# Kernel tuning notes

Measured on AMD Instinct MI355X. Metric: run time of the kernel, lower is better.

The kernel has to match this reference:

```python
import jax, jax.numpy as jnp
import numpy as np

B, C, W, H, D = 2, 256, 32, 32, 32
CH = C // 2  # 128
LN_EPS = 1e-5


def _spatial_pool(x, wm, bm):
    # x: [B,C,W,H,D]; wm: [C]; bm: scalar. 1x1x1 conv C->1 == channel dot.
    b, c = x.shape[0], x.shape[1]
    xf = x.reshape(b, c, -1)                       # [B,C,N]
    mask = jnp.einsum('bcn,c->bn', xf, wm) + bm    # [B,N]
    attn = jax.nn.softmax(mask, axis=1)            # softmax over spatial N
    return jnp.einsum('bcn,bn->bc', xf, attn)      # [B,C] weighted-sum pool


def _channel_add(ctx, w1, b1, g, be, w2, b2):
    # 1x1 conv C->C/2, LayerNorm over C/2, ReLU, 1x1 conv C/2->C
    h = ctx @ w1.T + b1                            # [B,CH]
    mu = jnp.mean(h, axis=-1, keepdims=True)
    var = jnp.mean((h - mu) ** 2, axis=-1, keepdims=True)
    h = (h - mu) * jax.lax.rsqrt(var + LN_EPS) * g + be
    h = jax.nn.relu(h)
    return h @ w2.T + b2                           # [B,C]


def setup_inputs() -> dict:
    key = jax.random.key(0)
    ks = jax.random.split(key, 20)
    s = 0.02
    d = {
        'preds_S': jax.random.normal(ks[0], (B, C, W, H, D), jnp.float32),
        'preds_T': jax.random.normal(ks[1], (B, C, W, H, D), jnp.float32),
        'wm_s': jax.random.normal(ks[2], (C,), jnp.float32) * s,
        'bm_s': jnp.zeros((), jnp.float32),
        'wm_t': jax.random.normal(ks[3], (C,), jnp.float32) * s,
        'bm_t': jnp.zeros((), jnp.float32),
        'w1_s': jax.random.normal(ks[4], (CH, C), jnp.float32) * s,
        'b1_s': jnp.zeros((CH,), jnp.float32),
        'g_s': jnp.ones((CH,), jnp.float32),
        'be_s': jnp.zeros((CH,), jnp.float32),
        'w2_s': jax.random.normal(ks[5], (C, CH), jnp.float32) * s,
        'b2_s': jnp.zeros((C,), jnp.float32),
        'w1_t': jax.random.normal(ks[6], (CH, C), jnp.float32) * s,
        'b1_t': jnp.zeros((CH,), jnp.float32),
        'g_t': jnp.ones((CH,), jnp.float32),
        'be_t': jnp.zeros((CH,), jnp.float32),
        'w2_t': jax.random.normal(ks[7], (C, CH), jnp.float32) * s,
        'b2_t': jnp.zeros((C,), jnp.float32),
    }
    return d


def reference(preds_S, preds_T, wm_s, bm_s, wm_t, bm_t,
              w1_s, b1_s, g_s, be_s, w2_s, b2_s,
              w1_t, b1_t, g_t, be_t, w2_t, b2_t):
    ctx_s = _spatial_pool(preds_S, wm_s, bm_s)     # [B,C]
    ctx_t = _spatial_pool(preds_T, wm_t, bm_t)
    add_s = _channel_add(ctx_s, w1_s, b1_s, g_s, be_s, w2_s, b2_s)  # [B,C]
    add_t = _channel_add(ctx_t, w1_t, b1_t, g_t, be_t, w2_t, b2_t)
    out_s = preds_S + add_s[:, :, None, None, None]
    out_t = preds_T + add_t[:, :, None, None, None]
    diff = out_s - out_t
    return jnp.sum(diff * diff) / preds_S.shape[0]
```

## Files before the change

kernel.cpp:

```cpp
#include <hip/hip_runtime.h>
#include <math.h>

#define Bc   2
#define Cc   256
#define Nn   32768
#define CHc  128
#define LN_EPS 1e-5f

#define TN    64
#define TPB   512
#define NQ    16
#define CG    32
#define CPG   8
#define GRIDX (Nn / TN)

__global__ __launch_bounds__(TPB, 2) void gc_fused(
    const float* __restrict__ S, const float* __restrict__ T,
    const float* __restrict__ wms, const float* __restrict__ bms,
    const float* __restrict__ wmt, const float* __restrict__ bmt,
    float* __restrict__ ctxnum,
    float* __restrict__ rowsum,
    float* __restrict__ den,
    float* __restrict__ sumsq) {
  const int b    = blockIdx.y;
  const int tid  = threadIdx.x;
  const int nq   = tid & (NQ - 1);
  const int cg   = tid >> 4;
  const int wv   = tid >> 6;
  const int lane = tid & 63;
  const int c0   = cg * CPG;
  const int n0   = blockIdx.x * TN + nq * 4;

  __shared__ float4 mredw[2][8][NQ];
  __shared__ float  cred[Cc * 17];
  __shared__ float  sqred[8];
  __shared__ float  denred[2][NQ];

  const float bS = bms[0];
  const float bT = bmt[0];

  const float* Sp = S + ((size_t)b * Cc + c0) * Nn + n0;
  const float* Tp = T + ((size_t)b * Cc + c0) * Nn + n0;

  float4 s4[CPG], t4[CPG];
#pragma unroll
  for (int i = 0; i < CPG; ++i) s4[i] = *(const float4*)(Sp + (size_t)i * Nn);
#pragma unroll
  for (int i = 0; i < CPG; ++i) t4[i] = *(const float4*)(Tp + (size_t)i * Nn);

  float wS[CPG], wT[CPG];
#pragma unroll
  for (int i = 0; i < CPG; ++i) { wS[i] = wms[c0 + i]; wT[i] = wmt[c0 + i]; }

  float4 ms = make_float4(0.f, 0.f, 0.f, 0.f);
  float4 mt = make_float4(0.f, 0.f, 0.f, 0.f);
#pragma unroll
  for (int i = 0; i < CPG; ++i) {
    ms.x += wS[i] * s4[i].x; ms.y += wS[i] * s4[i].y;
    ms.z += wS[i] * s4[i].z; ms.w += wS[i] * s4[i].w;
    mt.x += wT[i] * t4[i].x; mt.y += wT[i] * t4[i].y;
    mt.z += wT[i] * t4[i].z; mt.w += wT[i] * t4[i].w;
  }

#pragma unroll
  for (int m = 16; m <= 32; m <<= 1) {
    ms.x += __shfl_xor(ms.x, m); ms.y += __shfl_xor(ms.y, m);
    ms.z += __shfl_xor(ms.z, m); ms.w += __shfl_xor(ms.w, m);
    mt.x += __shfl_xor(mt.x, m); mt.y += __shfl_xor(mt.y, m);
    mt.z += __shfl_xor(mt.z, m); mt.w += __shfl_xor(mt.w, m);
  }
  if (lane < NQ) { mredw[0][wv][nq] = ms; mredw[1][wv][nq] = mt; }

  __syncthreads();

  float4 Ms = make_float4(0.f, 0.f, 0.f, 0.f);
  float4 Mt = make_float4(0.f, 0.f, 0.f, 0.f);
#pragma unroll
  for (int w = 0; w < 8; ++w) {
    const float4 a = mredw[0][w][nq];
    Ms.x += a.x; Ms.y += a.y; Ms.z += a.z; Ms.w += a.w;
    const float4 c = mredw[1][w][nq];
    Mt.x += c.x; Mt.y += c.y; Mt.z += c.z; Mt.w += c.w;
  }
  float4 es, et;
  es.x = __expf(Ms.x + bS); es.y = __expf(Ms.y + bS);
  es.z = __expf(Ms.z + bS); es.w = __expf(Ms.w + bS);
  et.x = __expf(Mt.x + bT); et.y = __expf(Mt.y + bT);
  et.z = __expf(Mt.z + bT); et.w = __expf(Mt.w + bT);

  if (tid < NQ) {
    denred[0][tid] = es.x + es.y + es.z + es.w;
    denred[1][tid] = et.x + et.y + et.z + et.w;
  }

#pragma unroll
  for (int i = 0; i < CPG; ++i)
    cred[(c0 + i) * 17 + nq] =
        s4[i].x * es.x + s4[i].y * es.y + s4[i].z * es.z + s4[i].w * es.w;
  __syncthreads();
  if (tid < Cc) {
    float a = 0.f;
#pragma unroll
    for (int k = 0; k < NQ; ++k) a += cred[tid * 17 + k];
    atomicAdd(&ctxnum[((size_t)0 * Bc + b) * Cc + tid], a);
  } else if (tid == Cc + 1) {
    float a = 0.f, c = 0.f;
#pragma unroll
    for (int k = 0; k < NQ; ++k) { a += denred[0][k]; c += denred[1][k]; }
    atomicAdd(&den[0 * Bc + b], a);
    atomicAdd(&den[1 * Bc + b], c);
  }
  __syncthreads();

#pragma unroll
  for (int i = 0; i < CPG; ++i)
    cred[(c0 + i) * 17 + nq] =
        t4[i].x * et.x + t4[i].y * et.y + t4[i].z * et.z + t4[i].w * et.w;
  __syncthreads();
  if (tid < Cc) {
    float c = 0.f;
#pragma unroll
    for (int k = 0; k < NQ; ++k) c += cred[tid * 17 + k];
    atomicAdd(&ctxnum[((size_t)1 * Bc + b) * Cc + tid], c);
  }
  __syncthreads();

  float sq = 0.f;
#pragma unroll
  for (int i = 0; i < CPG; ++i) {
    const float dx = s4[i].x - t4[i].x, dy = s4[i].y - t4[i].y;
    const float dz = s4[i].z - t4[i].z, dw = s4[i].w - t4[i].w;
    cred[(c0 + i) * 17 + nq] = dx + dy + dz + dw;
    sq += dx * dx + dy * dy + dz * dz + dw * dw;
  }
#pragma unroll
  for (int m = 1; m < 64; m <<= 1) sq += __shfl_xor(sq, m);
  if (lane == 0) sqred[wv] = sq;
  __syncthreads();
  if (tid < Cc) {
    float r = 0.f;
#pragma unroll
    for (int k = 0; k < NQ; ++k) r += cred[tid * 17 + k];
    atomicAdd(&rowsum[(size_t)b * Cc + tid], r);
  } else if (tid == Cc) {
    float v = 0.f;
#pragma unroll
    for (int w = 0; w < 8; ++w) v += sqred[w];
    atomicAdd(sumsq, v);
  }
}

__global__ __launch_bounds__(1024) void gc_k4a_mlp(
    const float* __restrict__ ctxr, const float* __restrict__ den,
    const float* __restrict__ w1s, const float* __restrict__ b1s,
    const float* __restrict__ gs,  const float* __restrict__ bes,
    const float* __restrict__ w2s, const float* __restrict__ b2s,
    const float* __restrict__ w1t, const float* __restrict__ b1t,
    const float* __restrict__ gt,  const float* __restrict__ bet,
    const float* __restrict__ w2t, const float* __restrict__ b2t,
    float* __restrict__ addv) {
  const int tt  = blockIdx.x >> 1;
  const int b   = blockIdx.x & 1;
  const int tid = threadIdx.x;

  const float* w1 = tt ? w1t : w1s;
  const float* b1 = tt ? b1t : b1s;
  const float* g  = tt ? gt  : gs;
  const float* be = tt ? bet : bes;
  const float* w2 = tt ? w2t : w2s;
  const float* b2 = tt ? b2t : b2s;

  __shared__ float cxs[Cc];
  __shared__ float part[1024];
  __shared__ float hbuf[CHc];
  __shared__ float hr[CHc];
  __shared__ float2 red2[128];
  __shared__ float mu_s, rstd_s;

  if (tid < Cc)
    cxs[tid] = ctxr[((size_t)tt * Bc + b) * Cc + tid] / den[tt * Bc + b];
  __syncthreads();

  {
    const int j = tid >> 3, s = tid & 7;
    const float* wr = w1 + j * Cc + s * 32;
    const float4* cx4 = (const float4*)(cxs + s * 32);
    float acc = 0.f;
#pragma unroll
    for (int k = 0; k < 8; ++k) {
      const float4 w = *(const float4*)(wr + k * 4);
      const float4 x = cx4[k];
      acc += w.x * x.x + w.y * x.y + w.z * x.z + w.w * x.w;
    }
    part[tid] = acc;
  }
  __syncthreads();
  if (tid < CHc) {
    float h = b1[tid];
#pragma unroll
    for (int q = 0; q < 8; ++q) h += part[tid * 8 + q];
    hbuf[tid] = h;
  }
  __syncthreads();

  if (tid < CHc) {
    const float v = hbuf[tid];
    red2[tid] = make_float2(v, v * v);
  }
  __syncthreads();
  for (int s = 64; s > 0; s >>= 1) {
    if (tid < s) {
      red2[tid].x += red2[tid + s].x;
      red2[tid].y += red2[tid + s].y;
    }
    __syncthreads();
  }
  if (tid == 0) {
    const float mu = red2[0].x / (float)CHc;
    const float var = red2[0].y / (float)CHc - mu * mu;
    mu_s = mu;
    rstd_s = rsqrtf(var + LN_EPS);
  }
  __syncthreads();
  if (tid < CHc) {
    const float v = (hbuf[tid] - mu_s) * rstd_s * g[tid] + be[tid];
    hr[tid] = v > 0.f ? v : 0.f;
  }
  __syncthreads();

  {
    const int c = tid >> 2, q = tid & 3;
    const float* wr = w2 + c * CHc + q * 32;
    const float4* h4 = (const float4*)(hr + q * 32);
    float acc = 0.f;
#pragma unroll
    for (int k = 0; k < 8; ++k) {
      const float4 w = *(const float4*)(wr + k * 4);
      const float4 x = h4[k];
      acc += w.x * x.x + w.y * x.y + w.z * x.z + w.w * x.w;
    }
    part[tid] = acc;
  }
  __syncthreads();
  if (tid < Cc) {
    float acc = b2[tid];
#pragma unroll
    for (int q = 0; q < 4; ++q) acc += part[tid * 4 + q];
    addv[((size_t)tt * Bc + b) * Cc + tid] = acc;
  }
}

__global__ __launch_bounds__(256) void gc_k4b_final(
    const float* __restrict__ addv, const float* __restrict__ rowsum,
    const float* __restrict__ sumsq, float* __restrict__ out) {
  const int tid = threadIdx.x;
  __shared__ float red[256];
  float part = 0.f;
  for (int job = tid; job < Bc * Cc; job += 256) {
    const int c = job & (Cc - 1);
    const int b = job >> 8;
    const float delta = addv[((size_t)0 * Bc + b) * Cc + c] -
                        addv[((size_t)1 * Bc + b) * Cc + c];
    part += 2.f * delta * rowsum[(size_t)b * Cc + c] +
            (float)Nn * delta * delta;
  }
  red[tid] = part;
  __syncthreads();
  for (int s = 128; s > 0; s >>= 1) {
    if (tid < s) red[tid] += red[tid + s];
    __syncthreads();
  }
  if (tid == 0) out[0] = (red[0] + sumsq[0]) / (float)Bc;
}

extern "C" void kernel_launch(void* const* d_in, const int* in_sizes, int n_in,
                              void* d_out, int out_size, void* d_ws,
                              size_t ws_size, hipStream_t stream) {
  const float* S   = (const float*)d_in[0];
  const float* T   = (const float*)d_in[1];
  const float* wms = (const float*)d_in[2];
  const float* bms = (const float*)d_in[3];
  const float* wmt = (const float*)d_in[4];
  const float* bmt = (const float*)d_in[5];
  const float* w1s = (const float*)d_in[6];
  const float* b1s = (const float*)d_in[7];
  const float* gs  = (const float*)d_in[8];
  const float* bes = (const float*)d_in[9];
  const float* w2s = (const float*)d_in[10];
  const float* b2s = (const float*)d_in[11];
  const float* w1t = (const float*)d_in[12];
  const float* b1t = (const float*)d_in[13];
  const float* gt  = (const float*)d_in[14];
  const float* bet = (const float*)d_in[15];
  const float* w2t = (const float*)d_in[16];
  const float* b2t = (const float*)d_in[17];
  float* out = (float*)d_out;

  float* ws     = (float*)d_ws;
  float* ctxnum = ws;
  float* rowsum = ctxnum + 2 * Bc * Cc;
  float* den    = rowsum + Bc * Cc;
  float* sumsq  = den + 4;
  float* addv   = sumsq + 1;

  hipMemsetAsync(d_ws, 0, (2 * Bc * Cc + Bc * Cc + 4 + 1) * sizeof(float),
                 stream);

  gc_fused<<<dim3(GRIDX, Bc), TPB, 0, stream>>>(S, T, wms, bms, wmt, bmt,
                                                ctxnum, rowsum, den, sumsq);
  gc_k4a_mlp<<<4, 1024, 0, stream>>>(ctxnum, den, w1s, b1s, gs, bes, w2s, b2s,
                                     w1t, b1t, gt, bet, w2t, b2t, addv);
  gc_k4b_final<<<1, 256, 0, stream>>>(addv, rowsum, sumsq, out);
}
```

Before: 207.9 us.

## Stage tiles via global_load_lds, loop per block, replace atomics with partial buffers

The main kernel now copies S and T tiles straight into LDS with global_load_lds. Each block loops over four spatial tiles and keeps its per-channel partial sums in registers. Each block then writes one row of partials to a workspace buffer, and the MLP and final kernels reduce those rows. This removes the global atomics and the workspace memset, cutting contention and a launch. The cost is synchronous LDS staging with no double buffering, a few more shuffles per channel, and serial reductions over 256 rows in small single-block kernels.

```diff
diff --git a/kernel.cpp b/kernel.cpp
--- a/kernel.cpp
+++ b/kernel.cpp
@@ -7,151 +7,153 @@
 #define CHc  128
 #define LN_EPS 1e-5f
 
-#define TN    64
-#define TPB   512
-#define NQ    16
-#define CG    32
-#define CPG   8
-#define GRIDX (Nn / TN)
-
-__global__ __launch_bounds__(TPB, 2) void gc_fused(
+#define TN    32
+#define TPT   4
+#define TPB   256
+#define NQ    8
+#define NB    (Nn / (TN * TPT))
+#define PR    772
+
+__device__ __forceinline__ void load_lds16(const float* g, float* l) {
+  __builtin_amdgcn_global_load_lds(
+      (const __attribute__((address_space(1))) void*)g,
+      (__attribute__((address_space(3))) void*)l, 16, 0, 0);
+}
+
+__global__ __launch_bounds__(TPB, 2) void gc_main(
     const float* __restrict__ S, const float* __restrict__ T,
     const float* __restrict__ wms, const float* __restrict__ bms,
     const float* __restrict__ wmt, const float* __restrict__ bmt,
-    float* __restrict__ ctxnum,
-    float* __restrict__ rowsum,
-    float* __restrict__ den,
-    float* __restrict__ sumsq) {
+    float* __restrict__ P) {
   const int b    = blockIdx.y;
+  const int blk  = blockIdx.x;
   const int tid  = threadIdx.x;
   const int nq   = tid & (NQ - 1);
-  const int cg   = tid >> 4;
+  const int cgrp = tid >> 3;
   const int wv   = tid >> 6;
   const int lane = tid & 63;
-  const int c0   = cg * CPG;
-  const int n0   = blockIdx.x * TN + nq * 4;
-
-  __shared__ float4 mredw[2][8][NQ];
-  __shared__ float  cred[Cc * 17];
-  __shared__ float  sqred[8];
-  __shared__ float  denred[2][NQ];
+  const int c0   = cgrp * 8;
+
+  __shared__ float  tileS[Cc * TN];
+  __shared__ float  tileT[Cc * TN];
+  __shared__ float4 mredw[2][4][NQ];
+  __shared__ float  sqred[4];
 
   const float bS = bms[0];
   const float bT = bmt[0];
 
-  const float* Sp = S + ((size_t)b * Cc + c0) * Nn + n0;
-  const float* Tp = T + ((size_t)b * Cc + c0) * Nn + n0;
-
-  float4 s4[CPG], t4[CPG];
-#pragma unroll
-  for (int i = 0; i < CPG; ++i) s4[i] = *(const float4*)(Sp + (size_t)i * Nn);
-#pragma unroll
-  for (int i = 0; i < CPG; ++i) t4[i] = *(const float4*)(Tp + (size_t)i * Nn);
-
-  float wS[CPG], wT[CPG];
-#pragma unroll
-  for (int i = 0; i < CPG; ++i) { wS[i] = wms[c0 + i]; wT[i] = wmt[c0 + i]; }
-
-  float4 ms = make_float4(0.f, 0.f, 0.f, 0.f);
-  float4 mt = make_float4(0.f, 0.f, 0.f, 0.f);
-#pragma unroll
-  for (int i = 0; i < CPG; ++i) {
-    ms.x += wS[i] * s4[i].x; ms.y += wS[i] * s4[i].y;
-    ms.z += wS[i] * s4[i].z; ms.w += wS[i] * s4[i].w;
-    mt.x += wT[i] * t4[i].x; mt.y += wT[i] * t4[i].y;
-    mt.z += wT[i] * t4[i].z; mt.w += wT[i] * t4[i].w;
-  }
-
-#pragma unroll
-  for (int m = 16; m <= 32; m <<= 1) {
-    ms.x += __shfl_xor(ms.x, m); ms.y += __shfl_xor(ms.y, m);
-    ms.z += __shfl_xor(ms.z, m); ms.w += __shfl_xor(ms.w, m);
-    mt.x += __shfl_xor(mt.x, m); mt.y += __shfl_xor(mt.y, m);
-    mt.z += __shfl_xor(mt.z, m); mt.w += __shfl_xor(mt.w, m);
-  }
-  if (lane < NQ) { mredw[0][wv][nq] = ms; mredw[1][wv][nq] = mt; }
-
-  __syncthreads();
-
-  float4 Ms = make_float4(0.f, 0.f, 0.f, 0.f);
-  float4 Mt = make_float4(0.f, 0.f, 0.f, 0.f);
-#pragma unroll
-  for (int w = 0; w < 8; ++w) {
-    const float4 a = mredw[0][w][nq];
-    Ms.x += a.x; Ms.y += a.y; Ms.z += a.z; Ms.w += a.w;
-    const float4 c = mredw[1][w][nq];
-    Mt.x += c.x; Mt.y += c.y; Mt.z += c.z; Mt.w += c.w;
-  }
-  float4 es, et;
-  es.x = __expf(Ms.x + bS); es.y = __expf(Ms.y + bS);
-  es.z = __expf(Ms.z + bS); es.w = __expf(Ms.w + bS);
-  et.x = __expf(Mt.x + bT); et.y = __expf(Mt.y + bT);
-  et.z = __expf(Mt.z + bT); et.w = __expf(Mt.w + bT);
-
-  if (tid < NQ) {
-    denred[0][tid] = es.x + es.y + es.z + es.w;
-    denred[1][tid] = et.x + et.y + et.z + et.w;
-  }
-
-#pragma unroll
-  for (int i = 0; i < CPG; ++i)
-    cred[(c0 + i) * 17 + nq] =
-        s4[i].x * es.x + s4[i].y * es.y + s4[i].z * es.z + s4[i].w * es.w;
-  __syncthreads();
-  if (tid < Cc) {
-    float a = 0.f;
-#pragma unroll
-    for (int k = 0; k < NQ; ++k) a += cred[tid * 17 + k];
-    atomicAdd(&ctxnum[((size_t)0 * Bc + b) * Cc + tid], a);
-  } else if (tid == Cc + 1) {
-    float a = 0.f, c = 0.f;
-#pragma unroll
-    for (int k = 0; k < NQ; ++k) { a += denred[0][k]; c += denred[1][k]; }
-    atomicAdd(&den[0 * Bc + b], a);
-    atomicAdd(&den[1 * Bc + b], c);
-  }
-  __syncthreads();
-
-#pragma unroll
-  for (int i = 0; i < CPG; ++i)
-    cred[(c0 + i) * 17 + nq] =
-        t4[i].x * et.x + t4[i].y * et.y + t4[i].z * et.z + t4[i].w * et.w;
-  __syncthreads();
-  if (tid < Cc) {
-    float c = 0.f;
-#pragma unroll
-    for (int k = 0; k < NQ; ++k) c += cred[tid * 17 + k];
-    atomicAdd(&ctxnum[((size_t)1 * Bc + b) * Cc + tid], c);
-  }
-  __syncthreads();
-
-  float sq = 0.f;
-#pragma unroll
-  for (int i = 0; i < CPG; ++i) {
-    const float dx = s4[i].x - t4[i].x, dy = s4[i].y - t4[i].y;
-    const float dz = s4[i].z - t4[i].z, dw = s4[i].w - t4[i].w;
-    cred[(c0 + i) * 17 + nq] = dx + dy + dz + dw;
-    sq += dx * dx + dy * dy + dz * dz + dw * dw;
-  }
-#pragma unroll
-  for (int m = 1; m < 64; m <<= 1) sq += __shfl_xor(sq, m);
-  if (lane == 0) sqred[wv] = sq;
-  __syncthreads();
-  if (tid < Cc) {
-    float r = 0.f;
-#pragma unroll
-    for (int k = 0; k < NQ; ++k) r += cred[tid * 17 + k];
-    atomicAdd(&rowsum[(size_t)b * Cc + tid], r);
-  } else if (tid == Cc) {
-    float v = 0.f;
-#pragma unroll
-    for (int w = 0; w < 8; ++w) v += sqred[w];
-    atomicAdd(sumsq, v);
-  }
-}
-
-__global__ __launch_bounds__(1024) void gc_k4a_mlp(
-    const float* __restrict__ ctxr, const float* __restrict__ den,
+  float wSv[8], wTv[8];
+#pragma unroll
+  for (int i = 0; i < 8; ++i) { wSv[i] = wms[c0 + i]; wTv[i] = wmt[c0 + i]; }
+
+  float acc_cs = 0.f, acc_ct = 0.f, acc_rs = 0.f, acc_sq = 0.f;
+  float acc_dens = 0.f, acc_dent = 0.f;
+
+  const int r = lane >> 3, o = lane & 7;
+
+  for (int it = 0; it < TPT; ++it) {
+    const int n0 = (blk * TPT + it) * TN;
+
+#pragma unroll
+    for (int j = 0; j < 16; ++j) {
+      const int ttn = j >> 3;
+      const int cb  = (wv * 8 + (j & 7)) * 8;
+      const float* gp = (ttn ? T : S) +
+          ((size_t)(b * Cc + cb + r)) * Nn + n0 + o * 4;
+      float* lp = (ttn ? tileT : tileS) + cb * TN;
+      load_lds16(gp, lp);
+    }
+    __syncthreads();
+
+    const float4* tS4 = (const float4*)tileS;
+    const float4* tT4 = (const float4*)tileT;
+
+    float4 ms = make_float4(0.f, 0.f, 0.f, 0.f);
+    float4 mt = make_float4(0.f, 0.f, 0.f, 0.f);
+#pragma unroll
+    for (int i = 0; i < 8; ++i) {
+      const float4 s = tS4[(c0 + i) * NQ + nq];
+      const float4 t = tT4[(c0 + i) * NQ + nq];
+      ms.x += wSv[i] * s.x; ms.y += wSv[i] * s.y;
+      ms.z += wSv[i] * s.z; ms.w += wSv[i] * s.w;
+      mt.x += wTv[i] * t.x; mt.y += wTv[i] * t.y;
+      mt.z += wTv[i] * t.z; mt.w += wTv[i] * t.w;
+    }
+#pragma unroll
+    for (int m = 8; m <= 32; m <<= 1) {
+      ms.x += __shfl_xor(ms.x, m); ms.y += __shfl_xor(ms.y, m);
+      ms.z += __shfl_xor(ms.z, m); ms.w += __shfl_xor(ms.w, m);
+      mt.x += __shfl_xor(mt.x, m); mt.y += __shfl_xor(mt.y, m);
+      mt.z += __shfl_xor(mt.z, m); mt.w += __shfl_xor(mt.w, m);
+    }
+    if (lane < NQ) { mredw[0][wv][nq] = ms; mredw[1][wv][nq] = mt; }
+    __syncthreads();
+
+    float4 Ms = make_float4(0.f, 0.f, 0.f, 0.f);
+    float4 Mt = make_float4(0.f, 0.f, 0.f, 0.f);
+#pragma unroll
+    for (int w = 0; w < 4; ++w) {
+      const float4 a = mredw[0][w][nq];
+      Ms.x += a.x; Ms.y += a.y; Ms.z += a.z; Ms.w += a.w;
+      const float4 c = mredw[1][w][nq];
+      Mt.x += c.x; Mt.y += c.y; Mt.z += c.z; Mt.w += c.w;
+    }
+    float4 es, et;
+    es.x = __expf(Ms.x + bS); es.y = __expf(Ms.y + bS);
+    es.z = __expf(Ms.z + bS); es.w = __expf(Ms.w + bS);
+    et.x = __expf(Mt.x + bT); et.y = __expf(Mt.y + bT);
+    et.z = __expf(Mt.z + bT); et.w = __expf(Mt.w + bT);
+    if (cgrp == 0) {
+      acc_dens += es.x + es.y + es.z + es.w;
+      acc_dent += et.x + et.y + et.z + et.w;
+    }
+
+#pragma unroll
+    for (int i = 0; i < 8; ++i) {
+      const float4 s = tS4[(c0 + i) * NQ + nq];
+      const float4 t = tT4[(c0 + i) * NQ + nq];
+      float cs = s.x * es.x + s.y * es.y + s.z * es.z + s.w * es.w;
+      float ct = t.x * et.x + t.y * et.y + t.z * et.z + t.w * et.w;
+      const float dx = s.x - t.x, dy = s.y - t.y;
+      const float dz = s.z - t.z, dw = s.w - t.w;
+      float rs = dx + dy + dz + dw;
+      acc_sq += dx * dx + dy * dy + dz * dz + dw * dw;
+#pragma unroll
+      for (int m = 1; m <= 4; m <<= 1) {
+        cs += __shfl_xor(cs, m);
+        ct += __shfl_xor(ct, m);
+        rs += __shfl_xor(rs, m);
+      }
+      if (nq == i) { acc_cs += cs; acc_ct += ct; acc_rs += rs; }
+    }
+    __syncthreads();
+  }
+
+#pragma unroll
+  for (int m = 1; m < 64; m <<= 1) acc_sq += __shfl_xor(acc_sq, m);
+  if (lane == 0) sqred[wv] = acc_sq;
+  if (wv == 0) {
+#pragma unroll
+    for (int m = 1; m <= 4; m <<= 1) {
+      acc_dens += __shfl_xor(acc_dens, m);
+      acc_dent += __shfl_xor(acc_dent, m);
+    }
+  }
+  __syncthreads();
+
+  float* Prow = P + ((size_t)b * NB + blk) * PR;
+  Prow[tid]       = acc_cs;
+  Prow[Cc + tid]  = acc_ct;
+  Prow[2 * Cc + tid] = acc_rs;
+  if (tid == 0) {
+    Prow[768] = acc_dens;
+    Prow[769] = acc_dent;
+    Prow[770] = sqred[0] + sqred[1] + sqred[2] + sqred[3];
+  }
+}
+
+__global__ __launch_bounds__(1024) void gc_mlp(
+    const float* __restrict__ P,
     const float* __restrict__ w1s, const float* __restrict__ b1s,
     const float* __restrict__ gs,  const float* __restrict__ bes,
     const float* __restrict__ w2s, const float* __restrict__ b2s,
@@ -170,6 +172,8 @@
   const float* w2 = tt ? w2t : w2s;
   const float* b2 = tt ? b2t : b2s;
 
+  __shared__ float red4[4][Cc];
+  __shared__ float den4[4];
   __shared__ float cxs[Cc];
   __shared__ float part[1024];
   __shared__ float hbuf[CHc];
@@ -177,8 +181,23 @@
   __shared__ float2 red2[128];
   __shared__ float mu_s, rstd_s;
 
+  {
+    const int c = tid & (Cc - 1), gq = tid >> 8;
+    float v = 0.f;
+    for (int t = gq * 64; t < gq * 64 + 64; ++t)
+      v += P[((size_t)b * NB + t) * PR + tt * Cc + c];
+    red4[gq][c] = v;
+    if (tid < 4) {
+      float dv = 0.f;
+      for (int t = tid * 64; t < tid * 64 + 64; ++t)
+        dv += P[((size_t)b * NB + t) * PR + 768 + tt];
+      den4[tid] = dv;
+    }
+  }
+  __syncthreads();
   if (tid < Cc)
-    cxs[tid] = ctxr[((size_t)tt * Bc + b) * Cc + tid] / den[tt * Bc + b];
+    cxs[tid] = (red4[0][tid] + red4[1][tid] + red4[2][tid] + red4[3][tid]) /
+               (den4[0] + den4[1] + den4[2] + den4[3]);
   __syncthreads();
 
   {
@@ -250,27 +269,53 @@
   }
 }
 
-__global__ __launch_bounds__(256) void gc_k4b_final(
-    const float* __restrict__ addv, const float* __restrict__ rowsum,
-    const float* __restrict__ sumsq, float* __restrict__ out) {
+__global__ __launch_bounds__(1024) void gc_fin(
+    const float* __restrict__ P, const float* __restrict__ addv,
+    float* __restrict__ out) {
   const int tid = threadIdx.x;
-  __shared__ float red[256];
+  __shared__ float rs2[2][2][Cc];
+  __shared__ float red[1024];
+  __shared__ float sq_tot;
+
+  {
+    const int c = tid & (Cc - 1), b = (tid >> 8) & 1, h = tid >> 9;
+    float v = 0.f;
+    for (int t = h * 128; t < h * 128 + 128; ++t)
+      v += P[((size_t)b * NB + t) * PR + 2 * Cc + c];
+    rs2[h][b][c] = v;
+  }
+  {
+    float sqv = 0.f;
+    if (tid < 512) {
+      const int b = tid >> 8, t = tid & (NB - 1);
+      sqv = P[((size_t)b * NB + t) * PR + 770];
+    }
+    red[tid] = sqv;
+  }
+  __syncthreads();
+  for (int s = 512; s > 0; s >>= 1) {
+    if (tid < s) red[tid] += red[tid + s];
+    __syncthreads();
+  }
+  if (tid == 0) sq_tot = red[0];
+  __syncthreads();
+
   float part = 0.f;
-  for (int job = tid; job < Bc * Cc; job += 256) {
-    const int c = job & (Cc - 1);
-    const int b = job >> 8;
+  if (tid < Bc * Cc) {
+    const int c = tid & (Cc - 1);
+    const int b = tid >> 8;
     const float delta = addv[((size_t)0 * Bc + b) * Cc + c] -
                         addv[((size_t)1 * Bc + b) * Cc + c];
-    part += 2.f * delta * rowsum[(size_t)b * Cc + c] +
-            (float)Nn * delta * delta;
+    const float rsum = rs2[0][b][c] + rs2[1][b][c];
+    part = 2.f * delta * rsum + (float)Nn * delta * delta;
   }
   red[tid] = part;
   __syncthreads();
-  for (int s = 128; s > 0; s >>= 1) {
+  for (int s = 512; s > 0; s >>= 1) {
     if (tid < s) red[tid] += red[tid + s];
     __syncthreads();
   }
-  if (tid == 0) out[0] = (red[0] + sumsq[0]) / (float)Bc;
+  if (tid == 0) out[0] = (red[0] + sq_tot) / (float)Bc;
 }
 
 extern "C" void kernel_launch(void* const* d_in, const int* in_sizes, int n_in,
@@ -296,19 +341,12 @@
   const float* b2t = (const float*)d_in[17];
   float* out = (float*)d_out;
 
-  float* ws     = (float*)d_ws;
-  float* ctxnum = ws;
-  float* rowsum = ctxnum + 2 * Bc * Cc;
-  float* den    = rowsum + Bc * Cc;
-  float* sumsq  = den + 4;
-  float* addv   = sumsq + 1;
-
-  hipMemsetAsync(d_ws, 0, (2 * Bc * Cc + Bc * Cc + 4 + 1) * sizeof(float),
-                 stream);
-
-  gc_fused<<<dim3(GRIDX, Bc), TPB, 0, stream>>>(S, T, wms, bms, wmt, bmt,
-                                                ctxnum, rowsum, den, sumsq);
-  gc_k4a_mlp<<<4, 1024, 0, stream>>>(ctxnum, den, w1s, b1s, gs, bes, w2s, b2s,
-                                     w1t, b1t, gt, bet, w2t, b2t, addv);
-  gc_k4b_final<<<1, 256, 0, stream>>>(addv, rowsum, sumsq, out);
-}
+  float* ws   = (float*)d_ws;
+  float* P    = ws;
+  float* addv = P + (size_t)2 * NB * PR;
+
+  gc_main<<<dim3(NB, Bc), TPB, 0, stream>>>(S, T, wms, bms, wmt, bmt, P);
+  gc_mlp<<<4, 1024, 0, stream>>>(P, w1s, b1s, gs, bes, w2s, b2s,
+                                 w1t, b1t, gt, bet, w2t, b2t, addv);
+  gc_fin<<<1, 1024, 0, stream>>>(P, addv, out);
+}
```

Measured after the change: 218.1 us. 4.9% more time.
